# Optimization experiments

Measured on AMD Instinct MI355X. Metric: run time of the kernel, lower is better.

The kernel has to match this reference:

```python
import jax, jax.numpy as jnp
import numpy as np

B, T, D, H = 2, 2048, 1024, 16
HD = D // H
SCALE = HD ** -0.5


def setup_inputs() -> dict:
    key = jax.random.key(0)
    k1, k2, k3 = jax.random.split(key, 3)
    x = jax.random.normal(k1, (B, T, D), dtype=jnp.float32)
    w_qkv = jax.random.normal(k2, (D, 3 * D), dtype=jnp.float32) * (D ** -0.5)
    w_proj = jax.random.normal(k3, (D, D), dtype=jnp.float32) * (D ** -0.5)
    b_proj = jnp.zeros((D,), dtype=jnp.float32)
    return {"x": x, "w_qkv": w_qkv, "w_proj": w_proj, "b_proj": b_proj}


def reference(x, w_qkv, w_proj, b_proj):
    b, t, d = x.shape
    qkv = jnp.einsum('btd,de->bte', x, w_qkv)            # [B,T,3D]
    qkv = qkv.reshape(b, t, 3, H, HD)
    q = qkv[:, :, 0].transpose(0, 2, 1, 3)               # [B,H,T,HD]
    k = qkv[:, :, 1].transpose(0, 2, 1, 3)
    v = qkv[:, :, 2].transpose(0, 2, 1, 3)
    scores = jnp.einsum('bhqd,bhkd->bhqk', q, k) * SCALE  # [B,H,T,T]
    # NOTE: faithful to the source, softmax over dim=1 (the HEAD axis)
    probs = jax.nn.softmax(scores, axis=1)
    attn_out = jnp.einsum('bhqk,bhkd->bhqd', probs, v)
    attn_out = attn_out.transpose(0, 2, 1, 3).reshape(b, t, d)
    out = jnp.einsum('btd,de->bte', attn_out, w_proj) + b_proj
    return out
```

## Files before the change

kernel.cpp:

```cpp
#include <hip/hip_runtime.h>
#include <hip/hip_bf16.h>
#include <stdint.h>

typedef __bf16 bf16;
typedef __attribute__((ext_vector_type(8))) __bf16 bf16x8;
typedef __attribute__((ext_vector_type(4))) __bf16 bf16x4;
typedef __attribute__((ext_vector_type(2))) __bf16 bf16x2;
typedef __attribute__((ext_vector_type(4))) float f32x4;

#define MFMA_16x16x32(a, b, c) __builtin_amdgcn_mfma_f32_16x16x32_bf16((a), (b), (c), 0, 0, 0)

__device__ __forceinline__ void gld_lds16(const void* g, void* l) {
    __builtin_amdgcn_global_load_lds(
        (const __attribute__((address_space(1))) void*)g,
        (__attribute__((address_space(3))) void*)l,
        16, 0, 0);
}

__global__ void cvt_f32_bf16(const float* __restrict__ in, bf16* __restrict__ out, int n) {
    int i = (blockIdx.x * blockDim.x + threadIdx.x) * 8;
    if (i >= n) return;
    f32x4 a = *(const f32x4*)(in + i);
    f32x4 b = *(const f32x4*)(in + i + 4);
    bf16x8 o;
#pragma unroll
    for (int j = 0; j < 4; ++j) { o[j] = (bf16)a[j]; o[j + 4] = (bf16)b[j]; }
    *(bf16x8*)(out + i) = o;
}

__global__ void transpose_cvt(const float* __restrict__ in, bf16* __restrict__ out, int R, int C) {
    __shared__ float tile[32][33];
    int c0 = blockIdx.x * 32, r0 = blockIdx.y * 32;
    int tc = threadIdx.x & 31, tr = threadIdx.x >> 5;
#pragma unroll
    for (int i = 0; i < 4; ++i) {
        int r = tr + i * 8;
        tile[r][tc] = in[(size_t)(r0 + r) * C + c0 + tc];
    }
    __syncthreads();
#pragma unroll
    for (int i = 0; i < 4; ++i) {
        int r = tr + i * 8;
        out[(size_t)(c0 + r) * R + r0 + tc] = (bf16)tile[tc][r];
    }
}

template <int EPI>
__global__ void __launch_bounds__(256) gemm_bf16(
    const bf16* __restrict__ A, const bf16* __restrict__ Bt, int M, int N, int K,
    float* __restrict__ Cf, const float* __restrict__ bias,
    bf16* __restrict__ q_out, bf16* __restrict__ k_out, bf16* __restrict__ v_out)
{
    __shared__ bf16 As[128 * 32];
    __shared__ bf16 Bs[128 * 32];
    const int t = threadIdx.x, w = t >> 6, l = t & 63;
    const int l15 = l & 15, lh = l >> 4;
    const int m0 = blockIdx.y * 128, n0 = blockIdx.x * 128;
    const int wm = w >> 1, wn = w & 1;

    const int srow = w * 16 + (l >> 2);
    const int scol = (l & 3) * 8;
    const bf16* gA = A + (size_t)(m0 + srow) * K + scol;
    const bf16* gB = Bt + (size_t)(n0 + srow) * K + scol;
    char* lA = (char*)As + w * 1024;
    char* lB = (char*)Bs + w * 1024;

    f32x4 acc[4][4] = {};

    for (int kt = 0; kt < K; kt += 32) {
        __syncthreads();
        gld_lds16(gA + kt, lA);
        gld_lds16(gA + (size_t)64 * K + kt, lA + 4096);
        gld_lds16(gB + kt, lB);
        gld_lds16(gB + (size_t)64 * K + kt, lB + 4096);
        asm volatile("s_waitcnt vmcnt(0)" ::: "memory");
        __syncthreads();

        const bf16* pa = As + (wm * 64 + l15) * 32 + lh * 8;
        const bf16* pb = Bs + (wn * 64 + l15) * 32 + lh * 8;
        bf16x8 af[4], bfr[4];
#pragma unroll
        for (int i = 0; i < 4; ++i) {
            af[i]  = *(const bf16x8*)(pa + i * 512);
            bfr[i] = *(const bf16x8*)(pb + i * 512);
        }
#pragma unroll
        for (int mi = 0; mi < 4; ++mi)
#pragma unroll
            for (int ni = 0; ni < 4; ++ni)
                acc[mi][ni] = MFMA_16x16x32(af[mi], bfr[ni], acc[mi][ni]);
    }

    if (EPI == 1) {
#pragma unroll
        for (int ni = 0; ni < 4; ++ni) {
            int n = n0 + wn * 64 + ni * 16 + l15;
            float bb = bias[n];
#pragma unroll
            for (int mi = 0; mi < 4; ++mi)
#pragma unroll
                for (int r = 0; r < 4; ++r) {
                    int m = m0 + wm * 64 + mi * 16 + lh * 4 + r;
                    Cf[(size_t)m * N + n] = acc[mi][ni][r] + bb;
                }
        }
    } else {
        const int which = n0 >> 10;
        const float QSCL = 0.125f * 1.44269504089f;
#pragma unroll
        for (int ni = 0; ni < 4; ++ni) {
            int n = n0 + wn * 64 + ni * 16 + l15;
            int h = (n >> 6) & 15;
            int d = n & 63;
#pragma unroll
            for (int mi = 0; mi < 4; ++mi)
#pragma unroll
                for (int r = 0; r < 4; ++r) {
                    int m = m0 + wm * 64 + mi * 16 + lh * 4 + r;
                    int b = m >> 11, tt = m & 2047;
                    float av = acc[mi][ni][r];
                    size_t hb = (size_t)b * 16 + h;
                    if (which == 0)      q_out[(hb * 2048 + tt) * 64 + d] = (bf16)(av * QSCL);
                    else if (which == 1) k_out[(hb * 2048 + tt) * 64 + d] = (bf16)av;
                    else                 v_out[(hb * 64 + d) * 2048 + tt] = (bf16)av;
                }
        }
    }
}

__global__ void __launch_bounds__(1024, 4) attn_kernel(
    const bf16* __restrict__ Q, const bf16* __restrict__ Kmat, const bf16* __restrict__ Vt,
    bf16* __restrict__ p0, bf16* __restrict__ p1, bf16* __restrict__ p2, bf16* __restrict__ p3)
{
    __shared__ bf16 S[2][16][32][72];
    __shared__ bf16 invS[32][72];
    const int t = threadIdx.x;
    const int w = t >> 6;
    const int l = t & 63;
    const int l15 = l & 15, lh = l >> 4;

    const int bid = blockIdx.x;
    const int b = (bid & 7) >> 2;
    const int ks = bid & 3;
    const int qt = (bid >> 3) * 32;

    const size_t headQK = ((size_t)b * 16 + w) * (2048 * 64);
    const size_t headV  = ((size_t)b * 16 + w) * (64 * 2048);

    bf16x8 qf[2][2];
#pragma unroll
    for (int qb2 = 0; qb2 < 2; ++qb2)
#pragma unroll
        for (int dc = 0; dc < 2; ++dc)
            qf[qb2][dc] = *(const bf16x8*)(Q + headQK + (size_t)(qt + qb2 * 16 + l15) * 64 + dc * 32 + lh * 8);

    f32x4 o[2][4] = {};

#define RAW_BARRIER() do { asm volatile("s_waitcnt lgkmcnt(0)" ::: "memory"); \
                           __builtin_amdgcn_s_barrier(); \
                           __builtin_amdgcn_sched_barrier(0); } while (0)

    auto SCORE = [&](int g, int buf) {
        const int kt = ks * 512 + g * 64;
#pragma unroll
        for (int kb = 0; kb < 4; ++kb) {
            const bf16* kp = Kmat + headQK + (size_t)(kt + kb * 16 + l15) * 64 + lh * 8;
            bf16x8 ak0 = *(const bf16x8*)(kp);
            bf16x8 ak1 = *(const bf16x8*)(kp + 32);
#pragma unroll
            for (int qb2 = 0; qb2 < 2; ++qb2) {
                f32x4 s = {};
                s = MFMA_16x16x32(ak0, qf[qb2][0], s);
                s = MFMA_16x16x32(ak1, qf[qb2][1], s);
                bf16x4 pk;
#pragma unroll
                for (int r = 0; r < 4; ++r)
                    pk[r] = (bf16)__builtin_amdgcn_exp2f(s[r]);
                *(bf16x4*)&S[buf][w][qb2 * 16 + l15][kb * 16 + lh * 4] = pk;
            }
        }
    };
    auto SUM = [&](int buf) {
        const int sq = t >> 5, kc = (t & 31) * 2;
        float s0 = 0.f, s1 = 0.f;
#pragma unroll
        for (int hh = 0; hh < 16; ++hh) {
            bf16x2 pr = *(const bf16x2*)&S[buf][hh][sq][kc];
            s0 += (float)pr[0]; s1 += (float)pr[1];
        }
        bf16x2 iv;
        iv[0] = (bf16)__builtin_amdgcn_rcpf(s0);
        iv[1] = (bf16)__builtin_amdgcn_rcpf(s1);
        *(bf16x2*)&invS[sq][kc] = iv;
    };
    auto PV = [&](int g, int buf) {
        const int kt = ks * 512 + g * 64;
#pragma unroll
        for (int ksub = 0; ksub < 2; ++ksub) {
            bf16x8 bv[4];
#pragma unroll
            for (int ni = 0; ni < 4; ++ni)
                bv[ni] = *(const bf16x8*)(Vt + headV + (size_t)(ni * 16 + l15) * 2048 + kt + ksub * 32 + lh * 8);
#pragma unroll
            for (int qb2 = 0; qb2 < 2; ++qb2) {
                bf16x8 ev  = *(const bf16x8*)(&S[buf][w][qb2 * 16 + l15][ksub * 32 + lh * 8]);
                bf16x8 ivv = *(const bf16x8*)(&invS[qb2 * 16 + l15][ksub * 32 + lh * 8]);
                bf16x8 ap;
#pragma unroll
                for (int j = 0; j < 8; ++j)
                    ap[j] = (bf16)((float)ev[j] * (float)ivv[j]);
                __builtin_amdgcn_s_setprio(1);
#pragma unroll
                for (int ni = 0; ni < 4; ++ni)
                    o[qb2][ni] = MFMA_16x16x32(ap, bv[ni], o[qb2][ni]);
                __builtin_amdgcn_s_setprio(0);
            }
        }
    };

    SCORE(0, 0);
    RAW_BARRIER();
    SUM(0);
    RAW_BARRIER();
#pragma unroll
    for (int g = 1; g < 8; ++g) {
        PV(g - 1, (g - 1) & 1);
        SCORE(g, g & 1);
        RAW_BARRIER();
        SUM(g & 1);
        RAW_BARRIER();
    }
    PV(7, 1);

#undef RAW_BARRIER

    bf16* dst = (ks == 0 ? p0 : ks == 1 ? p1 : ks == 2 ? p2 : p3) + (size_t)b * (2048 * 1024);
#pragma unroll
    for (int qb2 = 0; qb2 < 2; ++qb2)
#pragma unroll
        for (int ni = 0; ni < 4; ++ni)
#pragma unroll
            for (int r = 0; r < 4; ++r) {
                int tt = qt + qb2 * 16 + lh * 4 + r;
                int d = ni * 16 + l15;
                dst[(size_t)tt * 1024 + w * 64 + d] = (bf16)o[qb2][ni][r];
            }
}

__global__ void reduce_part4(const bf16* __restrict__ p0, const bf16* __restrict__ p1,
                             const bf16* __restrict__ p2, const bf16* __restrict__ p3,
                             bf16* __restrict__ out, int n) {
    int i = (blockIdx.x * blockDim.x + threadIdx.x) * 8;
    if (i >= n) return;
    bf16x8 a = *(const bf16x8*)(p0 + i);
    bf16x8 b = *(const bf16x8*)(p1 + i);
    bf16x8 c = *(const bf16x8*)(p2 + i);
    bf16x8 d = *(const bf16x8*)(p3 + i);
    bf16x8 o;
#pragma unroll
    for (int j = 0; j < 8; ++j)
        o[j] = (bf16)(((float)a[j] + (float)b[j]) + ((float)c[j] + (float)d[j]));
    *(bf16x8*)(out + i) = o;
}

extern "C" void kernel_launch(void* const* d_in, const int* in_sizes, int n_in,
                              void* d_out, int out_size, void* d_ws, size_t ws_size,
                              hipStream_t stream)
{
    const float* x      = (const float*)d_in[0];
    const float* w_qkv  = (const float*)d_in[1];
    const float* w_proj = (const float*)d_in[2];
    const float* b_proj = (const float*)d_in[3];
    float* out = (float*)d_out;

    char* ws = (char*)d_ws;
    const size_t MB = 1048576;
    bf16* wprojT = (bf16*)(ws + 0 * MB);
    bf16* xb     = (bf16*)(ws + 2 * MB);
    bf16* wqkvT  = (bf16*)(ws + 10 * MB);
    bf16* qb     = (bf16*)(ws + 18 * MB);
    bf16* kb     = (bf16*)(ws + 26 * MB);
    bf16* vt     = (bf16*)(ws + 34 * MB);
    bf16* part0  = (bf16*)(ws + 2 * MB);
    bf16* part1  = (bf16*)(ws + 10 * MB);
    bf16* part2  = (bf16*)(ws + 42 * MB);
    bf16* part3  = (bf16*)(ws + 50 * MB);
    bf16* attnb  = (bf16*)(ws + 2 * MB);

    cvt_f32_bf16<<<2048, 256, 0, stream>>>(x, xb, 4194304);
    transpose_cvt<<<dim3(96, 32), 256, 0, stream>>>(w_qkv, wqkvT, 1024, 3072);
    transpose_cvt<<<dim3(32, 32), 256, 0, stream>>>(w_proj, wprojT, 1024, 1024);

    gemm_bf16<0><<<dim3(24, 32), 256, 0, stream>>>(xb, wqkvT, 4096, 3072, 1024,
                                                   nullptr, nullptr, qb, kb, vt);
    attn_kernel<<<512, 1024, 0, stream>>>(qb, kb, vt, part0, part1, part2, part3);
    reduce_part4<<<2048, 256, 0, stream>>>(part0, part1, part2, part3, attnb, 4194304);
    gemm_bf16<1><<<dim3(8, 32), 256, 0, stream>>>(attnb, wprojT, 4096, 1024, 1024,
                                                  out, b_proj, nullptr, nullptr, nullptr);

    (void)in_sizes; (void)n_in; (void)out_size; (void)ws_size;
}
```

Before: 231.2 us.

## Fuse partial-sum reduction into projection GEMM and vectorize V-transpose stores

Removes the separate reduce_part4 kernel by having the output projection GEMM load the four attention partial buffers, sum them in registers and write the bf16 sum to LDS as its A tile. The QKV GEMM is specialized, and its transposed-V epilogue now writes four consecutive time steps as one bf16x4 store instead of scalar strided stores. This saves one launch and the write and re-read of the reduced activation. In exchange, each projection block re-reads the partials for every column tile (8x redundant loads), and the A path now uses synchronous register loads instead of async LDS loads.

```diff
diff --git a/kernel.cpp b/kernel.cpp
--- a/kernel.cpp
+++ b/kernel.cpp
@@ -45,10 +45,8 @@
     }
 }
 
-template <int EPI>
-__global__ void __launch_bounds__(256) gemm_bf16(
+__global__ void __launch_bounds__(256) gemm_qkv(
     const bf16* __restrict__ A, const bf16* __restrict__ Bt, int M, int N, int K,
-    float* __restrict__ Cf, const float* __restrict__ bias,
     bf16* __restrict__ q_out, bf16* __restrict__ k_out, bf16* __restrict__ v_out)
 {
     __shared__ bf16 As[128 * 32];
@@ -91,22 +89,25 @@
                 acc[mi][ni] = MFMA_16x16x32(af[mi], bfr[ni], acc[mi][ni]);
     }
 
-    if (EPI == 1) {
+    const int which = n0 >> 10;
+    const float QSCL = 0.125f * 1.44269504089f;
+    if (which == 2) {
 #pragma unroll
         for (int ni = 0; ni < 4; ++ni) {
             int n = n0 + wn * 64 + ni * 16 + l15;
-            float bb = bias[n];
-#pragma unroll
-            for (int mi = 0; mi < 4; ++mi)
-#pragma unroll
-                for (int r = 0; r < 4; ++r) {
-                    int m = m0 + wm * 64 + mi * 16 + lh * 4 + r;
-                    Cf[(size_t)m * N + n] = acc[mi][ni][r] + bb;
-                }
+            int h = (n >> 6) & 15;
+            int d = n & 63;
+#pragma unroll
+            for (int mi = 0; mi < 4; ++mi) {
+                int m = m0 + wm * 64 + mi * 16 + lh * 4;
+                int b = m >> 11, ttb = m & 2047;
+                bf16x4 v4;
+#pragma unroll
+                for (int r = 0; r < 4; ++r) v4[r] = (bf16)acc[mi][ni][r];
+                *(bf16x4*)&v_out[(((size_t)b * 16 + h) * 64 + d) * 2048 + ttb] = v4;
+            }
         }
     } else {
-        const int which = n0 >> 10;
-        const float QSCL = 0.125f * 1.44269504089f;
 #pragma unroll
         for (int ni = 0; ni < 4; ++ni) {
             int n = n0 + wn * 64 + ni * 16 + l15;
@@ -120,11 +121,79 @@
                     int b = m >> 11, tt = m & 2047;
                     float av = acc[mi][ni][r];
                     size_t hb = (size_t)b * 16 + h;
-                    if (which == 0)      q_out[(hb * 2048 + tt) * 64 + d] = (bf16)(av * QSCL);
-                    else if (which == 1) k_out[(hb * 2048 + tt) * 64 + d] = (bf16)av;
-                    else                 v_out[(hb * 64 + d) * 2048 + tt] = (bf16)av;
+                    if (which == 0) q_out[(hb * 2048 + tt) * 64 + d] = (bf16)(av * QSCL);
+                    else            k_out[(hb * 2048 + tt) * 64 + d] = (bf16)av;
                 }
         }
+    }
+}
+
+__global__ void __launch_bounds__(256) gemm2_fused(
+    const bf16* __restrict__ P0, const bf16* __restrict__ P1,
+    const bf16* __restrict__ P2, const bf16* __restrict__ P3,
+    const bf16* __restrict__ Bt, float* __restrict__ Cf, const float* __restrict__ bias)
+{
+    const int K = 1024, N = 1024;
+    __shared__ bf16 As[128 * 32];
+    __shared__ bf16 Bs[128 * 32];
+    const int t = threadIdx.x, w = t >> 6, l = t & 63;
+    const int l15 = l & 15, lh = l >> 4;
+    const int m0 = blockIdx.y * 128, n0 = blockIdx.x * 128;
+    const int wm = w >> 1, wn = w & 1;
+
+    const int srow = w * 16 + (l >> 2);
+    const int scol = (l & 3) * 8;
+    const bf16* gB = Bt + (size_t)(n0 + srow) * K + scol;
+    char* lB = (char*)Bs + w * 1024;
+
+    f32x4 acc[4][4] = {};
+
+    for (int kt = 0; kt < K; kt += 32) {
+        __syncthreads();
+        gld_lds16(gB + kt, lB);
+        gld_lds16(gB + (size_t)64 * K + kt, lB + 4096);
+#pragma unroll
+        for (int half = 0; half < 2; ++half) {
+            size_t off = (size_t)(m0 + half * 64 + srow) * K + kt + scol;
+            bf16x8 a0 = *(const bf16x8*)(P0 + off);
+            bf16x8 a1 = *(const bf16x8*)(P1 + off);
+            bf16x8 a2 = *(const bf16x8*)(P2 + off);
+            bf16x8 a3 = *(const bf16x8*)(P3 + off);
+            bf16x8 s;
+#pragma unroll
+            for (int j = 0; j < 8; ++j)
+                s[j] = (bf16)(((float)a0[j] + (float)a1[j]) + ((float)a2[j] + (float)a3[j]));
+            *(bf16x8*)(As + half * 2048 + t * 8) = s;
+        }
+        asm volatile("s_waitcnt vmcnt(0)" ::: "memory");
+        __syncthreads();
+
+        const bf16* pa = As + (wm * 64 + l15) * 32 + lh * 8;
+        const bf16* pb = Bs + (wn * 64 + l15) * 32 + lh * 8;
+        bf16x8 af[4], bfr[4];
+#pragma unroll
+        for (int i = 0; i < 4; ++i) {
+            af[i]  = *(const bf16x8*)(pa + i * 512);
+            bfr[i] = *(const bf16x8*)(pb + i * 512);
+        }
+#pragma unroll
+        for (int mi = 0; mi < 4; ++mi)
+#pragma unroll
+            for (int ni = 0; ni < 4; ++ni)
+                acc[mi][ni] = MFMA_16x16x32(af[mi], bfr[ni], acc[mi][ni]);
+    }
+
+#pragma unroll
+    for (int ni = 0; ni < 4; ++ni) {
+        int n = n0 + wn * 64 + ni * 16 + l15;
+        float bb = bias[n];
+#pragma unroll
+        for (int mi = 0; mi < 4; ++mi)
+#pragma unroll
+            for (int r = 0; r < 4; ++r) {
+                int m = m0 + wm * 64 + mi * 16 + lh * 4 + r;
+                Cf[(size_t)m * N + n] = acc[mi][ni][r] + bb;
+            }
     }
 }
 
@@ -245,22 +314,6 @@
                 int d = ni * 16 + l15;
                 dst[(size_t)tt * 1024 + w * 64 + d] = (bf16)o[qb2][ni][r];
             }
-}
-
-__global__ void reduce_part4(const bf16* __restrict__ p0, const bf16* __restrict__ p1,
-                             const bf16* __restrict__ p2, const bf16* __restrict__ p3,
-                             bf16* __restrict__ out, int n) {
-    int i = (blockIdx.x * blockDim.x + threadIdx.x) * 8;
-    if (i >= n) return;
-    bf16x8 a = *(const bf16x8*)(p0 + i);
-    bf16x8 b = *(const bf16x8*)(p1 + i);
-    bf16x8 c = *(const bf16x8*)(p2 + i);
-    bf16x8 d = *(const bf16x8*)(p3 + i);
-    bf16x8 o;
-#pragma unroll
-    for (int j = 0; j < 8; ++j)
-        o[j] = (bf16)(((float)a[j] + (float)b[j]) + ((float)c[j] + (float)d[j]));
-    *(bf16x8*)(out + i) = o;
 }
 
 extern "C" void kernel_launch(void* const* d_in, const int* in_sizes, int n_in,
@@ -285,18 +338,15 @@
     bf16* part1  = (bf16*)(ws + 10 * MB);
     bf16* part2  = (bf16*)(ws + 42 * MB);
     bf16* part3  = (bf16*)(ws + 50 * MB);
-    bf16* attnb  = (bf16*)(ws + 2 * MB);
 
     cvt_f32_bf16<<<2048, 256, 0, stream>>>(x, xb, 4194304);
     transpose_cvt<<<dim3(96, 32), 256, 0, stream>>>(w_qkv, wqkvT, 1024, 3072);
     transpose_cvt<<<dim3(32, 32), 256, 0, stream>>>(w_proj, wprojT, 1024, 1024);
 
-    gemm_bf16<0><<<dim3(24, 32), 256, 0, stream>>>(xb, wqkvT, 4096, 3072, 1024,
-                                                   nullptr, nullptr, qb, kb, vt);
+    gemm_qkv<<<dim3(24, 32), 256, 0, stream>>>(xb, wqkvT, 4096, 3072, 1024, qb, kb, vt);
     attn_kernel<<<512, 1024, 0, stream>>>(qb, kb, vt, part0, part1, part2, part3);
-    reduce_part4<<<2048, 256, 0, stream>>>(part0, part1, part2, part3, attnb, 4194304);
-    gemm_bf16<1><<<dim3(8, 32), 256, 0, stream>>>(attnb, wprojT, 4096, 1024, 1024,
-                                                  out, b_proj, nullptr, nullptr, nullptr);
+    gemm2_fused<<<dim3(8, 32), 256, 0, stream>>>(part0, part1, part2, part3,
+                                                 wprojT, out, b_proj);
 
     (void)in_sizes; (void)n_in; (void)out_size; (void)ws_size;
 }
```

New measurement: 262.5 us. 13.5% more time.
